# Kernel tuning notes

Measured on AMD Instinct MI355X. Metric: run time of the kernel, lower is better.

The kernel has to match this reference:

```python
import jax, jax.numpy as jnp
import numpy as np

EMBED_DIM = 128
HEADS = 4
HEAD_DIM = EMBED_DIM // HEADS
HIDDEN = EMBED_DIM * 4


def setup_inputs() -> dict:
    key = jax.random.key(0)
    ks = jax.random.split(key, 12)
    s = 0.02
    return {
        "x": jax.random.normal(ks[0], (4, 4096, EMBED_DIM), dtype=jnp.float32),
        "ln1_g": jnp.ones((EMBED_DIM,), jnp.float32),
        "ln1_b": jnp.zeros((EMBED_DIM,), jnp.float32),
        "qkv_w": jax.random.normal(ks[1], (EMBED_DIM, 3 * EMBED_DIM), jnp.float32) * s,
        "qkv_b": jnp.zeros((3 * EMBED_DIM,), jnp.float32),
        "proj_w": jax.random.normal(ks[2], (EMBED_DIM, EMBED_DIM), jnp.float32) * s,
        "proj_b": jnp.zeros((EMBED_DIM,), jnp.float32),
        "ln2_g": jnp.ones((EMBED_DIM,), jnp.float32),
        "ln2_b": jnp.zeros((EMBED_DIM,), jnp.float32),
        "mlp_w1": jax.random.normal(ks[3], (EMBED_DIM, HIDDEN), jnp.float32) * s,
        "mlp_b1": jnp.zeros((HIDDEN,), jnp.float32),
        "mlp_w2": jax.random.normal(ks[4], (HIDDEN, EMBED_DIM), jnp.float32) * s,
        "mlp_b2": jnp.zeros((EMBED_DIM,), jnp.float32),
    }


def _layernorm(x, g, b, eps=1e-5):
    mu = jnp.mean(x, axis=-1, keepdims=True)
    var = jnp.var(x, axis=-1, keepdims=True)
    return (x - mu) * jax.lax.rsqrt(var + eps) * g + b


def _msa(x, qkv_w, qkv_b, proj_w, proj_b):
    B, N, C = x.shape
    qkv = x @ qkv_w + qkv_b                       # [B,N,3C]
    qkv = qkv.reshape(B, N, 3, HEADS, HEAD_DIM)
    q, k, v = jnp.moveaxis(qkv, 2, 0)             # each [B,N,H,D]
    # scores: [B,H,N,N]
    attn = jnp.einsum("bnhd,bmhd->bhnm", q, k) / jnp.sqrt(jnp.float32(HEAD_DIM))
    attn = jax.nn.softmax(attn, axis=-1)
    out = jnp.einsum("bhnm,bmhd->bnhd", attn, v).reshape(B, N, C)
    return out @ proj_w + proj_b


def reference(x, ln1_g, ln1_b, qkv_w, qkv_b, proj_w, proj_b,
              ln2_g, ln2_b, mlp_w1, mlp_b1, mlp_w2, mlp_b2):
    # dropout is identity in eval mode
    x = x + _msa(_layernorm(x, ln1_g, ln1_b), qkv_w, qkv_b, proj_w, proj_b)
    h = _layernorm(x, ln2_g, ln2_b)
    h = jax.nn.gelu(h @ mlp_w1 + mlp_b1, approximate=False)
    x = x + (h @ mlp_w2 + mlp_b2)
    return x
```

## Files before the change

### kernel.cpp

```cpp
#include <hip/hip_runtime.h>
#include <hip/hip_bf16.h>
#include <math.h>

#define NSEQ   4096
#define CDIM   128
#define HD     32

typedef __attribute__((ext_vector_type(8))) short short8;
typedef __attribute__((ext_vector_type(4))) short short4v;
typedef __attribute__((ext_vector_type(4))) float f32x4;

#define QSCL (0.17677669529663687f * 1.4426950408889634f)

__device__ inline unsigned short f2bf(float f){
  union { float f; unsigned u; } v; v.f = f;
  return (unsigned short)((v.u + 0x7fffu + ((v.u >> 16) & 1u)) >> 16);
}
__device__ inline float bf2f(unsigned short u){
  union { unsigned u; float f; } v; v.u = ((unsigned)u) << 16;
  return v.f;
}
__device__ inline void gload_lds16(const unsigned short* g, unsigned short* l){
  __builtin_amdgcn_global_load_lds(
      (const __attribute__((address_space(1))) void*)g,
      (__attribute__((address_space(3))) void*)l, 16, 0, 0);
}


__global__ __launch_bounds__(256) void k_pack(
    const float* __restrict__ qkv_w, const float* __restrict__ qkv_b,
    const float* __restrict__ proj_w, const float* __restrict__ mlp_w1,
    const float* __restrict__ mlp_w2, unsigned short* __restrict__ wpack,
    float* __restrict__ bqs)
{
  const int gt = blockIdx.x * 256 + threadIdx.x;
  const int tile = gt >> 6, lane = gt & 63;
  const float* src; int N, KT, toff, dstoff; float scale = 1.f;
  if (tile < 96)       { src = qkv_w;  N = 384; KT = 4;  toff = tile;       dstoff = 0; }
  else if (tile < 128) { src = proj_w; N = 128; KT = 4;  toff = tile - 96;  dstoff = 49152; }
  else if (tile < 256) { src = mlp_w1; N = 512; KT = 4;  toff = tile - 128; dstoff = 65536; }
  else                 { src = mlp_w2; N = 128; KT = 16; toff = tile - 256; dstoff = 131072; }
  const int ct = toff / KT, kt = toff % KT;
  if (tile < 96 && ct < 8) scale = QSCL;
  const int row0 = kt * 32 + (lane >> 4) * 8, col = ct * 16 + (lane & 15);
  short8 v;
  #pragma unroll
  for (int i = 0; i < 8; i++)
    v[i] = (short)f2bf(src[(size_t)(row0 + i) * N + col] * scale);
  *(short8*)(wpack + dstoff + ((size_t)(ct * KT + kt) * 64 + lane) * 8) = v;
  if (gt < 384) bqs[gt] = qkv_b[gt] * (gt < 128 ? QSCL : 1.f);
}

__global__ __launch_bounds__(512) void k_qkv(
    const float* __restrict__ x, const float* __restrict__ g,
    const float* __restrict__ b, const unsigned short* __restrict__ wpack,
    const float* __restrict__ bqs, unsigned short* __restrict__ qkv)
{
  __shared__ unsigned short xn[64 * 128];
  const int tid = threadIdx.x;
  const int tok0 = blockIdx.x * 64;
  {
    const int grp = tid >> 5, l = tid & 31;
    #pragma unroll
    for (int it = 0; it < 4; it++){
      const int t = it * 16 + grp;
      const float4 xv = *(const float4*)(x + (size_t)(tok0 + t) * 128 + l * 4);
      float s  = xv.x + xv.y + xv.z + xv.w;
      float s2 = xv.x*xv.x + xv.y*xv.y + xv.z*xv.z + xv.w*xv.w;
      #pragma unroll
      for (int m = 1; m <= 16; m <<= 1){ s += __shfl_xor(s, m); s2 += __shfl_xor(s2, m); }
      const float mu = s * (1.f/128.f);
      const float rs = rsqrtf(s2 * (1.f/128.f) - mu*mu + 1e-5f);
      const int e = l * 4;
      const float4 gv = *(const float4*)(g + e), bv = *(const float4*)(b + e);
      short4v pk;
      pk[0] = (short)f2bf((xv.x - mu)*rs*gv.x + bv.x);
      pk[1] = (short)f2bf((xv.y - mu)*rs*gv.y + bv.y);
      pk[2] = (short)f2bf((xv.z - mu)*rs*gv.z + bv.z);
      pk[3] = (short)f2bf((xv.w - mu)*rs*gv.w + bv.w);
      const int bl = l >> 1;
      const int slot = bl * 64 + (t & 48) + ((t & 15) ^ bl);
      *(short4v*)(xn + slot * 8 + (l & 1) * 4) = pk;
    }
  }
  __syncthreads();
  const int wv = tid >> 6, lane = tid & 63, r = lane & 15, cg = lane >> 4;
  const int rt = wv & 3, ct0 = (wv >> 2) * 12;
  short8 af[4];
  #pragma unroll
  for (int kt = 0; kt < 4; kt++){
    const int bl = kt * 4 + cg;
    const int slot = bl * 64 + rt * 16 + (r ^ bl);
    af[kt] = *(const short8*)(xn + slot * 8);
  }
  const int bidx = tok0 >> 12, nloc = (tok0 & (NSEQ - 1)) + rt * 16 + cg * 4;
  for (int ct = ct0; ct < ct0 + 12; ct++){
    f32x4 acc = {0.f, 0.f, 0.f, 0.f};
    const unsigned short* bp = wpack + ((size_t)(ct * 4) * 64 + lane) * 8;
    #pragma unroll
    for (int kt = 0; kt < 4; kt++)
      acc = __builtin_amdgcn_mfma_f32_16x16x32_bf16(af[kt], *(const short8*)(bp + kt * 512), acc, 0, 0, 0);
    const int col = ct * 16 + r;
    const float bi = bqs[col];
    if (ct < 8){
      const int cc = col & 127, h = cc >> 5, d = cc & 31;
      unsigned short* plane = qkv + ((size_t)bidx * 4 + h) * (NSEQ * HD);
      #pragma unroll
      for (int reg = 0; reg < 4; reg++)
        plane[(size_t)(nloc + reg) * HD + d] = f2bf(acc[reg] + bi);
    } else if (ct < 16){
      const int cc = col & 127, h = cc >> 5, d = cc & 31;
      unsigned short* plane = qkv + ((size_t)16 + bidx * 4 + h) * (NSEQ * HD);
      const int t16 = ((tok0 & (NSEQ - 1)) >> 4) + rt;
      #pragma unroll
      for (int reg = 0; reg < 4; reg++)
        plane[(size_t)t16 * 512 + (d >> 3) * 128 + (cg * 4 + reg) * 8 + (d & 7)]
            = f2bf(acc[reg] + bi);
    } else {
      const int vct = ct - 16, h = vct >> 1, half = vct & 1;
      unsigned short* plane = qkv + ((size_t)32 + bidx * 4 + h) * (NSEQ * HD);
      const size_t ntile = (size_t)((tok0 & (NSEQ - 1)) >> 5) + (rt >> 1);
      const size_t vo = (ntile * 2 + half) * 512 + lane * 8 + (rt & 1) * 4;
      short4v pk;
      #pragma unroll
      for (int reg = 0; reg < 4; reg++) pk[reg] = (short)f2bf(acc[reg] + bi);
      *(short4v*)(plane + vo) = pk;
    }
  }
}

#define PROC(tag, sa, sb, sc, sd, vva, vvb)                                    \
  {                                                                            \
    float pA##tag[4], pB##tag[4], pC##tag[4], pD##tag[4];                      \
    _Pragma("unroll")                                                          \
    for (int i = 0; i < 4; i++){                                               \
      pA##tag[i] = __builtin_amdgcn_exp2f(sa[i]);                              \
      pB##tag[i] = __builtin_amdgcn_exp2f(sb[i]);                              \
      pC##tag[i] = __builtin_amdgcn_exp2f(sc[i]);                              \
      pD##tag[i] = __builtin_amdgcn_exp2f(sd[i]);                              \
    }                                                                          \
    unsigned q0,q1,q2,q3,q4,q5,q6,q7;                                          \
    asm("v_cvt_pk_bf16_f32 %0, %1, %2" : "=v"(q0) : "v"(pA##tag[0]), "v"(pA##tag[1])); \
    asm("v_cvt_pk_bf16_f32 %0, %1, %2" : "=v"(q1) : "v"(pA##tag[2]), "v"(pA##tag[3])); \
    asm("v_cvt_pk_bf16_f32 %0, %1, %2" : "=v"(q2) : "v"(pB##tag[0]), "v"(pB##tag[1])); \
    asm("v_cvt_pk_bf16_f32 %0, %1, %2" : "=v"(q3) : "v"(pB##tag[2]), "v"(pB##tag[3])); \
    asm("v_cvt_pk_bf16_f32 %0, %1, %2" : "=v"(q4) : "v"(pC##tag[0]), "v"(pC##tag[1])); \
    asm("v_cvt_pk_bf16_f32 %0, %1, %2" : "=v"(q5) : "v"(pC##tag[2]), "v"(pC##tag[3])); \
    asm("v_cvt_pk_bf16_f32 %0, %1, %2" : "=v"(q6) : "v"(pD##tag[0]), "v"(pD##tag[1])); \
    asm("v_cvt_pk_bf16_f32 %0, %1, %2" : "=v"(q7) : "v"(pD##tag[2]), "v"(pD##tag[3])); \
    union { unsigned u[4]; short8 s; } pa_##tag, pb_##tag;                     \
    pa_##tag.u[0]=q0; pa_##tag.u[1]=q1; pa_##tag.u[2]=q2; pa_##tag.u[3]=q3;    \
    pb_##tag.u[0]=q4; pb_##tag.u[1]=q5; pb_##tag.u[2]=q6; pb_##tag.u[3]=q7;    \
    o00 = __builtin_amdgcn_mfma_f32_16x16x32_bf16(vva, pa_##tag.s, o00, 0, 0, 0); \
    o01 = __builtin_amdgcn_mfma_f32_16x16x32_bf16(vvb, pa_##tag.s, o01, 0, 0, 0); \
    o10 = __builtin_amdgcn_mfma_f32_16x16x32_bf16(vva, pb_##tag.s, o10, 0, 0, 0); \
    o11 = __builtin_amdgcn_mfma_f32_16x16x32_bf16(vvb, pb_##tag.s, o11, 0, 0, 0); \
    lacc0 = __builtin_amdgcn_mfma_f32_16x16x32_bf16(vones, pa_##tag.s, lacc0, 0, 0, 0); \
    lacc1 = __builtin_amdgcn_mfma_f32_16x16x32_bf16(vones, pb_##tag.s, lacc1, 0, 0, 0); \
  }

__global__ __launch_bounds__(512) void k_attn(
    const unsigned short* __restrict__ qkv, unsigned short* __restrict__ part_ob,
    float* __restrict__ part_l)
{
  __shared__ unsigned short sbuf[16384];
  const int tid = threadIdx.x;
  const int lane = tid & 63, wv = tid >> 6;
  const int id = blockIdx.x;
  const int xcd = id & 7, seq = id >> 3;
  const int bh = xcd * 2 + (seq >> 5);
  const int sub = seq & 31;
  const int chunk = sub >> 4;
  const int qbase = (sub & 15) * 256 + wv * 32;
  const int kv0 = chunk * 2048;
  const unsigned short* Q  = qkv + (size_t)bh * (NSEQ * HD);
  const unsigned short* Kc = qkv + (size_t)(16 + bh) * (NSEQ * HD) + (size_t)kv0 * HD;
  const unsigned short* Vc = qkv + (size_t)(32 + bh) * (NSEQ * HD) + (size_t)kv0 * HD;
  const int r = lane & 15, cg = lane >> 4;
  const short8 qf0 = *(const short8*)(Q + (size_t)(qbase + r) * HD + cg * 8);
  const short8 qf1 = *(const short8*)(Q + (size_t)(qbase + 16 + r) * HD + cg * 8);
  const unsigned short* gsrc = (wv < 4 ? Kc + wv * 512 : Vc + (wv - 4) * 512) + lane * 8;
  const int dst = wv * 512;
  union { unsigned u[4]; short8 s; } onesu;
  onesu.u[0] = 0x3F803F80u; onesu.u[1] = 0x3F803F80u;
  onesu.u[2] = 0x3F803F80u; onesu.u[3] = 0x3F803F80u;
  const short8 vones = onesu.s;
  f32x4 o00 = {0.f,0.f,0.f,0.f}, o01 = {0.f,0.f,0.f,0.f};
  f32x4 o10 = {0.f,0.f,0.f,0.f}, o11 = {0.f,0.f,0.f,0.f};
  f32x4 lacc0 = {0.f,0.f,0.f,0.f}, lacc1 = {0.f,0.f,0.f,0.f};
  const f32x4 zero = {0.f,0.f,0.f,0.f};
  gload_lds16(gsrc,        sbuf + 0 * 4096 + dst);
  gload_lds16(gsrc + 2048, sbuf + 1 * 4096 + dst);
  gload_lds16(gsrc + 4096, sbuf + 2 * 4096 + dst);
  f32x4 s0_00, s0_01, s0_10, s0_11, s1_00, s1_01, s1_10, s1_11;
  short8 vp00, vp01, vp10, vp11;
  asm volatile("s_waitcnt vmcnt(2) lgkmcnt(0)" ::: "memory");
  __builtin_amdgcn_sched_barrier(0);
  __builtin_amdgcn_s_barrier();
  __builtin_amdgcn_sched_barrier(0);
  gload_lds16(gsrc + 3 * 2048, sbuf + 3 * 4096 + dst);
  {
    const unsigned short* skb = sbuf;
    const unsigned short* svb = sbuf + 2048;
    const short8 ka0 = *(const short8*)(skb + 0 * 512 + lane * 8);
    const short8 ka1 = *(const short8*)(skb + 1 * 512 + lane * 8);
    const short8 ka2 = *(const short8*)(skb + 2 * 512 + lane * 8);
    const short8 ka3 = *(const short8*)(skb + 3 * 512 + lane * 8);
    vp00 = *(const short8*)(svb + 0 * 512 + lane * 8);
    vp01 = *(const short8*)(svb + 1 * 512 + lane * 8);
    vp10 = *(const short8*)(svb + 2 * 512 + lane * 8);
    vp11 = *(const short8*)(svb + 3 * 512 + lane * 8);
    s0_00 = __builtin_amdgcn_mfma_f32_16x16x32_bf16(ka0, qf0, zero, 0, 0, 0);
    s0_01 = __builtin_amdgcn_mfma_f32_16x16x32_bf16(ka1, qf0, zero, 0, 0, 0);
    s0_10 = __builtin_amdgcn_mfma_f32_16x16x32_bf16(ka0, qf1, zero, 0, 0, 0);
    s0_11 = __builtin_amdgcn_mfma_f32_16x16x32_bf16(ka1, qf1, zero, 0, 0, 0);
    s1_00 = __builtin_amdgcn_mfma_f32_16x16x32_bf16(ka2, qf0, zero, 0, 0, 0);
    s1_01 = __builtin_amdgcn_mfma_f32_16x16x32_bf16(ka3, qf0, zero, 0, 0, 0);
    s1_10 = __builtin_amdgcn_mfma_f32_16x16x32_bf16(ka2, qf1, zero, 0, 0, 0);
    s1_11 = __builtin_amdgcn_mfma_f32_16x16x32_bf16(ka3, qf1, zero, 0, 0, 0);
  }
  for (int t = 1; t < 32; t++){
    asm volatile("s_waitcnt vmcnt(2) lgkmcnt(0)" ::: "memory");
    __builtin_amdgcn_sched_barrier(0);
    __builtin_amdgcn_s_barrier();
    __builtin_amdgcn_sched_barrier(0);
    const int tn = (t + 3 > 31) ? 31 : t + 3;
    gload_lds16(gsrc + (size_t)tn * 2048, sbuf + ((t + 3) & 3) * 4096 + dst);
    const unsigned short* skb = sbuf + (t & 3) * 4096;
    const unsigned short* svb = skb + 2048;
    const short8 ka0 = *(const short8*)(skb + 0 * 512 + lane * 8);
    const short8 ka1 = *(const short8*)(skb + 1 * 512 + lane * 8);
    const short8 ka2 = *(const short8*)(skb + 2 * 512 + lane * 8);
    const short8 ka3 = *(const short8*)(skb + 3 * 512 + lane * 8);
    const short8 nv00 = *(const short8*)(svb + 0 * 512 + lane * 8);
    const short8 nv01 = *(const short8*)(svb + 1 * 512 + lane * 8);
    const short8 nv10 = *(const short8*)(svb + 2 * 512 + lane * 8);
    const short8 nv11 = *(const short8*)(svb + 3 * 512 + lane * 8);
    PROC(a, s0_00, s0_01, s0_10, s0_11, vp00, vp01)
    PROC(b, s1_00, s1_01, s1_10, s1_11, vp10, vp11)
    s0_00 = __builtin_amdgcn_mfma_f32_16x16x32_bf16(ka0, qf0, zero, 0, 0, 0);
    s0_01 = __builtin_amdgcn_mfma_f32_16x16x32_bf16(ka1, qf0, zero, 0, 0, 0);
    s0_10 = __builtin_amdgcn_mfma_f32_16x16x32_bf16(ka0, qf1, zero, 0, 0, 0);
    s0_11 = __builtin_amdgcn_mfma_f32_16x16x32_bf16(ka1, qf1, zero, 0, 0, 0);
    s1_00 = __builtin_amdgcn_mfma_f32_16x16x32_bf16(ka2, qf0, zero, 0, 0, 0);
    s1_01 = __builtin_amdgcn_mfma_f32_16x16x32_bf16(ka3, qf0, zero, 0, 0, 0);
    s1_10 = __builtin_amdgcn_mfma_f32_16x16x32_bf16(ka2, qf1, zero, 0, 0, 0);
    s1_11 = __builtin_amdgcn_mfma_f32_16x16x32_bf16(ka3, qf1, zero, 0, 0, 0);
    vp00 = nv00; vp01 = nv01; vp10 = nv10; vp11 = nv11;
  }
  PROC(c, s0_00, s0_01, s0_10, s0_11, vp00, vp01)
  PROC(d, s1_00, s1_01, s1_10, s1_11, vp10, vp11)
  asm volatile("s_waitcnt vmcnt(0)" ::: "memory");
  const float ls0 = lacc0[0], ls1 = lacc1[0];
  unsigned short* po = part_ob + (((size_t)(chunk * 16 + bh) * NSEQ) + qbase + r) * HD;
  short4v w0, w1, w2, w3;
  #pragma unroll
  for (int j = 0; j < 4; j++){
    w0[j] = (short)f2bf(o00[j]); w1[j] = (short)f2bf(o01[j]);
    w2[j] = (short)f2bf(o10[j]); w3[j] = (short)f2bf(o11[j]);
  }
  *(short4v*)(po + cg * 4)              = w0;
  *(short4v*)(po + 16 + cg * 4)         = w1;
  *(short4v*)(po + 16 * HD + cg * 4)    = w2;
  *(short4v*)(po + 16 * HD + 16 + cg * 4) = w3;
  if (lane < 16){
    part_l[(size_t)(chunk * 16 + bh) * NSEQ + qbase + r] = ls0;
    part_l[(size_t)(chunk * 16 + bh) * NSEQ + qbase + 16 + r] = ls1;
  }
}
#undef PROC

__global__ __launch_bounds__(512, 6) void k_fused(
    const unsigned short* __restrict__ part_ob, const float* __restrict__ part_l,
    const float* __restrict__ x, const unsigned short* __restrict__ wpack,
    const float* __restrict__ pb, const float* __restrict__ g2,
    const float* __restrict__ b2, const float* __restrict__ b1,
    const float* __restrict__ b2m, float* __restrict__ out)
{
  __shared__ unsigned short afh[2][2048];
  __shared__ unsigned short sbb[32 * 128];
  __shared__ unsigned short afr[2][8192];
  const int tid = threadIdx.x, tok0 = blockIdx.x * 32;
  const int wv = tid >> 6, lane = tid & 63, r = lane & 15, cg = lane >> 4;
  const int rt = wv & 1, cgp = wv >> 1;
  const int bidx = tok0 >> 12;
  {
    const int row = tid >> 4;
    const int c0 = (tid & 15) * 8;
    const int kt = c0 >> 5, cgf = (c0 >> 3) & 3;
    const int bh = bidx * 4 + kt;
    const size_t q = (size_t)((tok0 & (NSEQ - 1)) + row);
    float s8[8] = {0.f,0.f,0.f,0.f,0.f,0.f,0.f,0.f};
    float lsum = 0.f;
    #pragma unroll
    for (int c = 0; c < 2; c++){
      const short8 v = *(const short8*)(part_ob +
          (((size_t)(c * 16 + bh) * NSEQ) + q) * HD + (c0 & 31));
      #pragma unroll
      for (int i = 0; i < 8; i++) s8[i] += bf2f((unsigned short)v[i]);
      lsum += part_l[(size_t)(c * 16 + bh) * NSEQ + q];
    }
    const float inv = 1.f / lsum;
    short8 pk;
    #pragma unroll
    for (int i = 0; i < 8; i++) pk[i] = (short)f2bf(s8[i] * inv);
    *(short8*)(&afh[row >> 4][(kt * 4 + cgf) * 128 + (row & 15) * 8]) = pk;
  }
  __syncthreads();
  {
    short8 af[4];
    #pragma unroll
    for (int kt = 0; kt < 4; kt++)
      af[kt] = *(const short8*)(&afh[rt][(kt * 4 + cg) * 128 + r * 8]);
    const unsigned short* wp = wpack + 49152;
    for (int ct = cgp * 2; ct < cgp * 2 + 2; ct++){
      f32x4 acc = {0.f, 0.f, 0.f, 0.f};
      const unsigned short* bp = wp + ((size_t)(ct * 4) * 64 + lane) * 8;
      #pragma unroll
      for (int kt = 0; kt < 4; kt++)
        acc = __builtin_amdgcn_mfma_f32_16x16x32_bf16(af[kt], *(const short8*)(bp + kt * 512), acc, 0, 0, 0);
      const int col = ct * 16 + r;
      const float bi = pb[col];
      #pragma unroll
      for (int reg = 0; reg < 4; reg++){
        const int tl = rt * 16 + cg * 4 + reg;
        sbb[tl * 128 + col] = f2bf(acc[reg] + bi + x[(size_t)(tok0 + tl) * 128 + col]);
      }
    }
  }
  __syncthreads();
  {
    const int grp = tid >> 5, l = tid & 31;
    #pragma unroll
    for (int it = 0; it < 2; it++){
      const int t = it * 16 + grp;
      const short4v xb = *(const short4v*)(sbb + t * 128 + l * 4);
      const float x0 = bf2f((unsigned short)xb[0]), x1 = bf2f((unsigned short)xb[1]);
      const float x2 = bf2f((unsigned short)xb[2]), x3 = bf2f((unsigned short)xb[3]);
      float s  = x0 + x1 + x2 + x3;
      float s2 = x0*x0 + x1*x1 + x2*x2 + x3*x3;
      #pragma unroll
      for (int m = 1; m <= 16; m <<= 1){ s += __shfl_xor(s, m); s2 += __shfl_xor(s2, m); }
      const float mu = s * (1.f/128.f);
      const float rs = rsqrtf(s2 * (1.f/128.f) - mu*mu + 1e-5f);
      const int e = l * 4;
      const float4 gv = *(const float4*)(g2 + e), bv = *(const float4*)(b2 + e);
      short4v pk;
      pk[0] = (short)f2bf((x0 - mu)*rs*gv.x + bv.x);
      pk[1] = (short)f2bf((x1 - mu)*rs*gv.y + bv.y);
      pk[2] = (short)f2bf((x2 - mu)*rs*gv.z + bv.z);
      pk[3] = (short)f2bf((x3 - mu)*rs*gv.w + bv.w);
      *(short4v*)(&afh[t >> 4][(e >> 3) * 128 + (t & 15) * 8 + (e & 7)]) = pk;
    }
  }
  __syncthreads();
  {
    short8 hf[4];
    #pragma unroll
    for (int kt = 0; kt < 4; kt++)
      hf[kt] = *(const short8*)(&afh[rt][(kt * 4 + cg) * 128 + r * 8]);
    const unsigned short* w1 = wpack + 65536;
    for (int ct = cgp * 8; ct < cgp * 8 + 8; ct++){
      f32x4 acc = {0.f, 0.f, 0.f, 0.f};
      const unsigned short* bp = w1 + ((size_t)(ct * 4) * 64 + lane) * 8;
      #pragma unroll
      for (int kt = 0; kt < 4; kt++)
        acc = __builtin_amdgcn_mfma_f32_16x16x32_bf16(hf[kt], *(const short8*)(bp + kt * 512), acc, 0, 0, 0);
      const int col = ct * 16 + r;
      const float bi = b1[col];
      #pragma unroll
      for (int reg = 0; reg < 4; reg++){
        const float v = acc[reg] + bi;
        const float u = v * (2.3022077f + 0.10294324f * v * v);
        const float ge = v * __builtin_amdgcn_rcpf(1.f + __builtin_amdgcn_exp2f(-u));
        afr[rt][(col >> 3) * 128 + (cg * 4 + reg) * 8 + (col & 7)] = f2bf(ge);
      }
    }
  }
  __syncthreads();
  {
    const unsigned short* w2 = wpack + 131072;
    f32x4 acc0 = {0.f,0.f,0.f,0.f}, acc1 = {0.f,0.f,0.f,0.f};
    for (int kt = 0; kt < 16; kt++){
      const short8 a3 = *(const short8*)(&afr[rt][(kt * 4 + cg) * 128 + r * 8]);
      const unsigned short* bp0 = w2 + ((size_t)((cgp * 2 + 0) * 16 + kt) * 64 + lane) * 8;
      const unsigned short* bp1 = w2 + ((size_t)((cgp * 2 + 1) * 16 + kt) * 64 + lane) * 8;
      acc0 = __builtin_amdgcn_mfma_f32_16x16x32_bf16(a3, *(const short8*)(bp0), acc0, 0, 0, 0);
      acc1 = __builtin_amdgcn_mfma_f32_16x16x32_bf16(a3, *(const short8*)(bp1), acc1, 0, 0, 0);
    }
    #pragma unroll
    for (int c = 0; c < 2; c++){
      const f32x4 acc = c ? acc1 : acc0;
      const int col = (cgp * 2 + c) * 16 + r;
      const float bi = b2m[col];
      #pragma unroll
      for (int reg = 0; reg < 4; reg++){
        const int tl = rt * 16 + cg * 4 + reg;
        out[(size_t)(tok0 + tl) * 128 + col] = acc[reg] + bi + bf2f(sbb[tl * 128 + col]);
      }
    }
  }
}

extern "C" void kernel_launch(void* const* d_in, const int* in_sizes, int n_in,
                              void* d_out, int out_size, void* d_ws, size_t ws_size,
                              hipStream_t stream)
{
  const float* x      = (const float*)d_in[0];
  const float* ln1_g  = (const float*)d_in[1];
  const float* ln1_b  = (const float*)d_in[2];
  const float* qkv_w  = (const float*)d_in[3];
  const float* qkv_b  = (const float*)d_in[4];
  const float* proj_w = (const float*)d_in[5];
  const float* proj_b = (const float*)d_in[6];
  const float* ln2_g  = (const float*)d_in[7];
  const float* ln2_b  = (const float*)d_in[8];
  const float* mlp_w1 = (const float*)d_in[9];
  const float* mlp_b1 = (const float*)d_in[10];
  const float* mlp_w2 = (const float*)d_in[11];
  const float* mlp_b2 = (const float*)d_in[12];

  char* ws = (char*)d_ws;
  unsigned short* wpack   = (unsigned short*)(ws);
  float*          bqs     = (float*)(ws + 393216);
  unsigned short* qkv     = (unsigned short*)(ws + 524288);
  unsigned short* part_ob = (unsigned short*)(ws + 13107200);
  float*          part_l  = (float*)(ws + 29884416);
  float* out = (float*)d_out;

  hipLaunchKernelGGL(k_pack, dim3(96), dim3(256), 0, stream,
                     qkv_w, qkv_b, proj_w, mlp_w1, mlp_w2, wpack, bqs);
  hipLaunchKernelGGL(k_qkv, dim3(256), dim3(512), 0, stream,
                     x, ln1_g, ln1_b, wpack, bqs, qkv);
  hipLaunchKernelGGL(k_attn, dim3(512), dim3(512), 0, stream,
                     qkv, part_ob, part_l);
  hipLaunchKernelGGL(k_fused, dim3(512), dim3(512), 0, stream,
                     part_ob, part_l, x, wpack, proj_b, ln2_g, ln2_b,
                     mlp_b1, mlp_b2, out);
}
```

Before: 79.47 us.

## Load K/V fragments directly from global memory instead of LDS staging

```diff
diff --git a/kernel.cpp b/kernel.cpp
--- a/kernel.cpp
+++ b/kernel.cpp
@@ -19,11 +19,6 @@
 __device__ inline float bf2f(unsigned short u){
   union { unsigned u; float f; } v; v.u = ((unsigned)u) << 16;
   return v.f;
-}
-__device__ inline void gload_lds16(const unsigned short* g, unsigned short* l){
-  __builtin_amdgcn_global_load_lds(
-      (const __attribute__((address_space(1))) void*)g,
-      (__attribute__((address_space(3))) void*)l, 16, 0, 0);
 }
 
 
@@ -163,7 +158,6 @@
     const unsigned short* __restrict__ qkv, unsigned short* __restrict__ part_ob,
     float* __restrict__ part_l)
 {
-  __shared__ unsigned short sbuf[16384];
   const int tid = threadIdx.x;
   const int lane = tid & 63, wv = tid >> 6;
   const int id = blockIdx.x;
@@ -174,13 +168,13 @@
   const int qbase = (sub & 15) * 256 + wv * 32;
   const int kv0 = chunk * 2048;
   const unsigned short* Q  = qkv + (size_t)bh * (NSEQ * HD);
-  const unsigned short* Kc = qkv + (size_t)(16 + bh) * (NSEQ * HD) + (size_t)kv0 * HD;
-  const unsigned short* Vc = qkv + (size_t)(32 + bh) * (NSEQ * HD) + (size_t)kv0 * HD;
   const int r = lane & 15, cg = lane >> 4;
   const short8 qf0 = *(const short8*)(Q + (size_t)(qbase + r) * HD + cg * 8);
   const short8 qf1 = *(const short8*)(Q + (size_t)(qbase + 16 + r) * HD + cg * 8);
-  const unsigned short* gsrc = (wv < 4 ? Kc + wv * 512 : Vc + (wv - 4) * 512) + lane * 8;
-  const int dst = wv * 512;
+  const unsigned short* kp = qkv + (size_t)(16 + bh) * (NSEQ * HD)
+                           + (size_t)kv0 * HD + lane * 8;
+  const unsigned short* vp = qkv + (size_t)(32 + bh) * (NSEQ * HD)
+                           + (size_t)kv0 * HD + lane * 8;
   union { unsigned u[4]; short8 s; } onesu;
   onesu.u[0] = 0x3F803F80u; onesu.u[1] = 0x3F803F80u;
   onesu.u[2] = 0x3F803F80u; onesu.u[3] = 0x3F803F80u;
@@ -189,27 +183,17 @@
   f32x4 o10 = {0.f,0.f,0.f,0.f}, o11 = {0.f,0.f,0.f,0.f};
   f32x4 lacc0 = {0.f,0.f,0.f,0.f}, lacc1 = {0.f,0.f,0.f,0.f};
   const f32x4 zero = {0.f,0.f,0.f,0.f};
-  gload_lds16(gsrc,        sbuf + 0 * 4096 + dst);
-  gload_lds16(gsrc + 2048, sbuf + 1 * 4096 + dst);
-  gload_lds16(gsrc + 4096, sbuf + 2 * 4096 + dst);
   f32x4 s0_00, s0_01, s0_10, s0_11, s1_00, s1_01, s1_10, s1_11;
   short8 vp00, vp01, vp10, vp11;
-  asm volatile("s_waitcnt vmcnt(2) lgkmcnt(0)" ::: "memory");
-  __builtin_amdgcn_sched_barrier(0);
-  __builtin_amdgcn_s_barrier();
-  __builtin_amdgcn_sched_barrier(0);
-  gload_lds16(gsrc + 3 * 2048, sbuf + 3 * 4096 + dst);
-  {
-    const unsigned short* skb = sbuf;
-    const unsigned short* svb = sbuf + 2048;
-    const short8 ka0 = *(const short8*)(skb + 0 * 512 + lane * 8);
-    const short8 ka1 = *(const short8*)(skb + 1 * 512 + lane * 8);
-    const short8 ka2 = *(const short8*)(skb + 2 * 512 + lane * 8);
-    const short8 ka3 = *(const short8*)(skb + 3 * 512 + lane * 8);
-    vp00 = *(const short8*)(svb + 0 * 512 + lane * 8);
-    vp01 = *(const short8*)(svb + 1 * 512 + lane * 8);
-    vp10 = *(const short8*)(svb + 2 * 512 + lane * 8);
-    vp11 = *(const short8*)(svb + 3 * 512 + lane * 8);
+  {
+    const short8 ka0 = *(const short8*)(kp + 0 * 512);
+    const short8 ka1 = *(const short8*)(kp + 1 * 512);
+    const short8 ka2 = *(const short8*)(kp + 2 * 512);
+    const short8 ka3 = *(const short8*)(kp + 3 * 512);
+    vp00 = *(const short8*)(vp + 0 * 512);
+    vp01 = *(const short8*)(vp + 1 * 512);
+    vp10 = *(const short8*)(vp + 2 * 512);
+    vp11 = *(const short8*)(vp + 3 * 512);
     s0_00 = __builtin_amdgcn_mfma_f32_16x16x32_bf16(ka0, qf0, zero, 0, 0, 0);
     s0_01 = __builtin_amdgcn_mfma_f32_16x16x32_bf16(ka1, qf0, zero, 0, 0, 0);
     s0_10 = __builtin_amdgcn_mfma_f32_16x16x32_bf16(ka0, qf1, zero, 0, 0, 0);
@@ -220,22 +204,16 @@
     s1_11 = __builtin_amdgcn_mfma_f32_16x16x32_bf16(ka3, qf1, zero, 0, 0, 0);
   }
   for (int t = 1; t < 32; t++){
-    asm volatile("s_waitcnt vmcnt(2) lgkmcnt(0)" ::: "memory");
-    __builtin_amdgcn_sched_barrier(0);
-    __builtin_amdgcn_s_barrier();
-    __builtin_amdgcn_sched_barrier(0);
-    const int tn = (t + 3 > 31) ? 31 : t + 3;
-    gload_lds16(gsrc + (size_t)tn * 2048, sbuf + ((t + 3) & 3) * 4096 + dst);
-    const unsigned short* skb = sbuf + (t & 3) * 4096;
-    const unsigned short* svb = skb + 2048;
-    const short8 ka0 = *(const short8*)(skb + 0 * 512 + lane * 8);
-    const short8 ka1 = *(const short8*)(skb + 1 * 512 + lane * 8);
-    const short8 ka2 = *(const short8*)(skb + 2 * 512 + lane * 8);
-    const short8 ka3 = *(const short8*)(skb + 3 * 512 + lane * 8);
-    const short8 nv00 = *(const short8*)(svb + 0 * 512 + lane * 8);
-    const short8 nv01 = *(const short8*)(svb + 1 * 512 + lane * 8);
-    const short8 nv10 = *(const short8*)(svb + 2 * 512 + lane * 8);
-    const short8 nv11 = *(const short8*)(svb + 3 * 512 + lane * 8);
+    const unsigned short* kpt = kp + (size_t)t * 2048;
+    const unsigned short* vpt = vp + (size_t)t * 2048;
+    const short8 ka0 = *(const short8*)(kpt + 0 * 512);
+    const short8 ka1 = *(const short8*)(kpt + 1 * 512);
+    const short8 ka2 = *(const short8*)(kpt + 2 * 512);
+    const short8 ka3 = *(const short8*)(kpt + 3 * 512);
+    const short8 nv00 = *(const short8*)(vpt + 0 * 512);
+    const short8 nv01 = *(const short8*)(vpt + 1 * 512);
+    const short8 nv10 = *(const short8*)(vpt + 2 * 512);
+    const short8 nv11 = *(const short8*)(vpt + 3 * 512);
     PROC(a, s0_00, s0_01, s0_10, s0_11, vp00, vp01)
     PROC(b, s1_00, s1_01, s1_10, s1_11, vp10, vp11)
     s0_00 = __builtin_amdgcn_mfma_f32_16x16x32_bf16(ka0, qf0, zero, 0, 0, 0);
@@ -250,7 +228,6 @@
   }
   PROC(c, s0_00, s0_01, s0_10, s0_11, vp00, vp01)
   PROC(d, s1_00, s1_01, s1_10, s1_11, vp10, vp11)
-  asm volatile("s_waitcnt vmcnt(0)" ::: "memory");
   const float ls0 = lacc0[0], ls1 = lacc1[0];
   unsigned short* po = part_ob + (((size_t)(chunk * 16 + bh) * NSEQ) + qbase + r) * HD;
   short4v w0, w1, w2, w3;
```

Result: no change. 80.06 us (+0.7%).
